# Optimization experiments

Hardware: AMD Instinct MI355X
Metric: run time of the kernel (lower is better)

## Reference

```python
import jax, jax.numpy as jnp
import numpy as np

# GeoFormer.generate_proposal constants (cfg.threshold_ins, cfg.min_pts_num,
# instance classes start at semantic id 4 on ScanNet)
THRESHOLD = 0.5
MIN_PTS_NUM = 50
MIN_INST_CLASS = 4


def setup_inputs() -> dict:
    key = jax.random.key(0)
    k1, k2, k3, k4 = jax.random.split(key, 4)
    B, Q, N, C = 4, 128, 50000, 20
    mask_logits = jax.random.normal(k1, (B, Q, N), dtype=jnp.float32)
    cls_logits = jax.random.normal(k2, (B, Q, C), dtype=jnp.float32)
    seg_pred = jax.random.randint(k3, (B, N), 0, C, dtype=jnp.int64)
    fg_idxs = jax.random.randint(k4, (B * N,), 0, 300000, dtype=jnp.int64)
    return {"mask_logits": mask_logits, "cls_logits": cls_logits,
            "seg_pred": seg_pred, "fg_idxs": fg_idxs}


def reference(mask_logits, cls_logits, seg_pred, fg_idxs):
    # mask_logits: [B, Q, N]  per-query point-mask logits (dense form of the
    #   per-batch list in the original; batch_offsets become the B dim)
    # cls_logits:  [B, Q, C]  per-query class logits
    # seg_pred:    [B, N]     per-point semantic prediction
    # fg_idxs:     [B*N]      foreground -> original point id map
    B, Q, N = mask_logits.shape
    m = jax.nn.sigmoid(mask_logits)                         # [B, Q, N]
    cls_pred = jnp.argmax(cls_logits, axis=2)               # [B, Q]

    # (mask_logit_b[n] > threshold) & (seg_pred == cls_logits_pred[b, n])
    sel = (m > THRESHOLD) & (seg_pred[:, None, :] == cls_pred[:, :, None])  # [B,Q,N]
    cnt = sel.sum(axis=-1)                                  # [B, Q] proposal sizes

    # score = mean of sigmoid over selected points
    msel = jnp.where(sel, m, jnp.zeros((), m.dtype))
    scores = msel.sum(axis=-1) / jnp.maximum(cnt, 1).astype(m.dtype)  # [B, Q]

    # skip if too few points or a background/wall class (< 4)
    valid = (cnt >= MIN_PTS_NUM) & (cls_pred >= MIN_INST_CLASS)       # [B, Q]

    proposal_masks = sel & valid[:, :, None]                # dense proposal_idx
    scores = jnp.where(valid, scores, jnp.zeros((), scores.dtype))
    global_ids = fg_idxs.reshape(B, N)                      # fg_idxs remap per point
    return proposal_masks, scores, valid, cls_pred, global_ids
```

## Files before the change

### kernel.cpp

```cpp
#include <hip/hip_runtime.h>
#include <math.h>

#define BB 4
#define QQ 128
#define NN 50000
#define CC 20
#define ROWS (BB * QQ)
#define NV4 (NN / 4)
#define TPB 256
#define BPR 4
#define QUOTA (NV4 / BPR)
#define FULL_ITERS 12
#define TAIL 53
#define THRESH_CNT 50
#define MIN_CLS 4

typedef float f32x4 __attribute__((ext_vector_type(4)));
typedef int   i32x4 __attribute__((ext_vector_type(4)));

struct Ws {
    float sum[ROWS];
    int   cnt[ROWS];
    int   cls[ROWS];
    int   valid[ROWS];
};

__global__ void k0_argmax_zero(const float* __restrict__ cls_logits, Ws* ws) {
    int r = blockIdx.x * blockDim.x + threadIdx.x;
    if (r >= ROWS) return;
    const float* p = cls_logits + r * CC;
    float best = p[0];
    int bi = 0;
    #pragma unroll
    for (int c = 1; c < CC; ++c) {
        float v = p[c];
        if (v > best) { best = v; bi = c; }
    }
    ws->cls[r] = bi;
    ws->sum[r] = 0.0f;
    ws->cnt[r] = 0;
}

__global__ __launch_bounds__(256) void k1_select(
        const float* __restrict__ mask_logits,
        const int*   __restrict__ seg_pred,
        float* __restrict__ out_mask,
        Ws* __restrict__ ws) {
    const int row = blockIdx.y;
    const int b   = row >> 7;
    const int cls = ws->cls[row];
    const int off = blockIdx.x * QUOTA;

    const f32x4* __restrict__ ml = (const f32x4*)(mask_logits + (size_t)row * NN) + off;
    const i32x4* __restrict__ sp = (const i32x4*)(seg_pred + b * NN) + off;
    f32x4* __restrict__ om = (f32x4*)(out_mask + (size_t)row * NN) + off;

    const int t = threadIdx.x;

    float lsum = 0.0f;
    int   lcnt = 0;

    f32x4 v0[4]; i32x4 s0v[4];
    #pragma unroll
    for (int j = 0; j < 4; ++j) {
        v0[j]  = ml[t + j * TPB];
        s0v[j] = sp[t + j * TPB];
    }

    #pragma unroll
    for (int bat = 0; bat < 3; ++bat) {
        f32x4 nv[4]; i32x4 ns[4];
        if (bat < 2) {
            const int nbase = (bat + 1) * (4 * TPB) + t;
            #pragma unroll
            for (int j = 0; j < 4; ++j) {
                nv[j] = ml[nbase + j * TPB];
                ns[j] = sp[nbase + j * TPB];
            }
        }
        const int base = bat * (4 * TPB) + t;
        #pragma unroll
        for (int j = 0; j < 4; ++j) {
            f32x4 vv = v0[j];
            i32x4 ss = s0v[j];
            bool c0 = (vv.x > 0.0f) & (ss.x == cls);
            bool c1 = (vv.y > 0.0f) & (ss.y == cls);
            bool c2 = (vv.z > 0.0f) & (ss.z == cls);
            bool c3 = (vv.w > 0.0f) & (ss.w == cls);
            float g0 = 1.0f / (1.0f + __expf(-vv.x));
            float g1 = 1.0f / (1.0f + __expf(-vv.y));
            float g2 = 1.0f / (1.0f + __expf(-vv.z));
            float g3 = 1.0f / (1.0f + __expf(-vv.w));
            f32x4 o;
            o.x = c0 ? 1.0f : 0.0f;
            o.y = c1 ? 1.0f : 0.0f;
            o.z = c2 ? 1.0f : 0.0f;
            o.w = c3 ? 1.0f : 0.0f;
            lsum += (c0 ? g0 : 0.0f) + (c1 ? g1 : 0.0f)
                  + (c2 ? g2 : 0.0f) + (c3 ? g3 : 0.0f);
            lcnt += (int)c0 + (int)c1 + (int)c2 + (int)c3;
            __builtin_nontemporal_store(o, &om[base + j * TPB]);
        }
        #pragma unroll
        for (int j = 0; j < 4; ++j) { v0[j] = nv[j]; s0v[j] = ns[j]; }
    }

    if (t < TAIL) {
        const int idx = FULL_ITERS * TPB + t;
        f32x4 vv = ml[idx];
        i32x4 ss = sp[idx];
        bool c0 = (vv.x > 0.0f) & (ss.x == cls);
        bool c1 = (vv.y > 0.0f) & (ss.y == cls);
        bool c2 = (vv.z > 0.0f) & (ss.z == cls);
        bool c3 = (vv.w > 0.0f) & (ss.w == cls);
        float g0 = 1.0f / (1.0f + __expf(-vv.x));
        float g1 = 1.0f / (1.0f + __expf(-vv.y));
        float g2 = 1.0f / (1.0f + __expf(-vv.z));
        float g3 = 1.0f / (1.0f + __expf(-vv.w));
        f32x4 o;
        o.x = c0 ? 1.0f : 0.0f;
        o.y = c1 ? 1.0f : 0.0f;
        o.z = c2 ? 1.0f : 0.0f;
        o.w = c3 ? 1.0f : 0.0f;
        lsum += (c0 ? g0 : 0.0f) + (c1 ? g1 : 0.0f)
              + (c2 ? g2 : 0.0f) + (c3 ? g3 : 0.0f);
        lcnt += (int)c0 + (int)c1 + (int)c2 + (int)c3;
        __builtin_nontemporal_store(o, &om[idx]);
    }

    #pragma unroll
    for (int offr = 32; offr > 0; offr >>= 1) {
        lsum += __shfl_down(lsum, offr);
        lcnt += __shfl_down(lcnt, offr);
    }
    __shared__ float ssum[4];
    __shared__ int   scnt[4];
    const int wave = threadIdx.x >> 6;
    const int lane = threadIdx.x & 63;
    if (lane == 0) { ssum[wave] = lsum; scnt[wave] = lcnt; }
    __syncthreads();
    if (threadIdx.x == 0) {
        float ts = ssum[0] + ssum[1] + ssum[2] + ssum[3];
        int   tc = scnt[0] + scnt[1] + scnt[2] + scnt[3];
        atomicAdd(&ws->sum[row], ts);
        atomicAdd(&ws->cnt[row], tc);
    }
}

__global__ void k2_finalize_gids(const int* __restrict__ fg,
                                 float* __restrict__ out,
                                 Ws* __restrict__ ws) {
    const int idx = blockIdx.x * blockDim.x + threadIdx.x;
    if (idx < ROWS) {
        int   cnt = ws->cnt[idx];
        int   cls = ws->cls[idx];
        float sum = ws->sum[idx];
        int valid = (cnt >= THRESH_CNT) && (cls >= MIN_CLS);
        ws->valid[idx] = valid;
        float* tail = out + (size_t)ROWS * NN;
        tail[idx]            = valid ? (sum / (float)max(cnt, 1)) : 0.0f;
        tail[ROWS + idx]     = valid ? 1.0f : 0.0f;
        tail[2 * ROWS + idx] = (float)cls;
    }
    const int nv4 = (BB * NN) / 4;
    if (idx < nv4) {
        float* gids = out + (size_t)ROWS * NN + 3 * ROWS;
        i32x4 v = ((const i32x4*)fg)[idx];
        f32x4 o;
        o.x = (float)v.x; o.y = (float)v.y; o.z = (float)v.z; o.w = (float)v.w;
        __builtin_nontemporal_store(o, &((f32x4*)gids)[idx]);
    }
}

__global__ __launch_bounds__(256) void k3_fixup(
        float* __restrict__ out_mask, const Ws* __restrict__ ws) {
    const int row = blockIdx.y;
    if (ws->valid[row]) return;
    f32x4* __restrict__ om = (f32x4*)(out_mask + (size_t)row * NN)
                             + blockIdx.x * QUOTA;
    const f32x4 z = {0.0f, 0.0f, 0.0f, 0.0f};
    const int t = threadIdx.x;
    #pragma unroll
    for (int i = 0; i < FULL_ITERS; ++i)
        __builtin_nontemporal_store(z, &om[t + i * TPB]);
    if (t < TAIL)
        __builtin_nontemporal_store(z, &om[FULL_ITERS * TPB + t]);
}

extern "C" void kernel_launch(void* const* d_in, const int* in_sizes, int n_in,
                              void* d_out, int out_size, void* d_ws, size_t ws_size,
                              hipStream_t stream) {
    const float* mask_logits = (const float*)d_in[0];
    const float* cls_logits  = (const float*)d_in[1];
    const int*   seg_pred    = (const int*)d_in[2];
    const int*   fg_idxs     = (const int*)d_in[3];

    float* out = (float*)d_out;
    Ws* ws = (Ws*)d_ws;

    float* out_mask = out;

    k0_argmax_zero<<<(ROWS + 255) / 256, 256, 0, stream>>>(cls_logits, ws);

    dim3 g1(BPR, ROWS);
    k1_select<<<g1, TPB, 0, stream>>>(mask_logits, seg_pred, out_mask, ws);

    const int gids_blocks = ((BB * NN) / 4 + 255) / 256;
    k2_finalize_gids<<<gids_blocks, 256, 0, stream>>>(fg_idxs, out, ws);

    k3_fixup<<<g1, TPB, 0, stream>>>(out_mask, ws);
}
```

Baseline: 204.4 us.

## Compact selection masks to ballot bitmasks and write final masks once

The first pass now computes the argmax inline, produces per-wave ballot bitmasks of the selection in workspace, and stores per-block partial sums instead of using atomics. A second pass reads the bits and the validity flag and writes the full float mask exactly once. This removes the dense write followed by a zero-fixup rewrite for invalid rows, and the separate argmax launch. It depends on the workspace being large enough, and otherwise falls back to the old path. Nontemporal stores are replaced by plain stores.

```diff
diff --git a/kernel.cpp b/kernel.cpp
--- a/kernel.cpp
+++ b/kernel.cpp
@@ -14,9 +14,20 @@
 #define TAIL 53
 #define THRESH_CNT 50
 #define MIN_CLS 4
+#define NITER 13
 
 typedef float f32x4 __attribute__((ext_vector_type(4)));
 typedef int   i32x4 __attribute__((ext_vector_type(4)));
+typedef unsigned long long u64;
+typedef unsigned long long u64x2 __attribute__((ext_vector_type(2)));
+
+struct Ws2 {
+    float psum[ROWS][BPR];
+    int   pcnt[ROWS][BPR];
+    int   cls[ROWS];
+    int   valid[ROWS];
+    u64   bits[(size_t)ROWS * BPR * NITER * 16];
+};
 
 struct Ws {
     float sum[ROWS];
@@ -25,84 +36,63 @@
     int   valid[ROWS];
 };
 
-__global__ void k0_argmax_zero(const float* __restrict__ cls_logits, Ws* ws) {
-    int r = blockIdx.x * blockDim.x + threadIdx.x;
-    if (r >= ROWS) return;
-    const float* p = cls_logits + r * CC;
-    float best = p[0];
-    int bi = 0;
-    #pragma unroll
-    for (int c = 1; c < CC; ++c) {
-        float v = p[c];
-        if (v > best) { best = v; bi = c; }
-    }
-    ws->cls[r] = bi;
-    ws->sum[r] = 0.0f;
-    ws->cnt[r] = 0;
-}
-
-__global__ __launch_bounds__(256) void k1_select(
+
+__global__ __launch_bounds__(256) void k1a_reduce_bits(
         const float* __restrict__ mask_logits,
         const int*   __restrict__ seg_pred,
-        float* __restrict__ out_mask,
-        Ws* __restrict__ ws) {
+        const float* __restrict__ cls_logits,
+        Ws2* __restrict__ ws) {
     const int row = blockIdx.y;
     const int b   = row >> 7;
-    const int cls = ws->cls[row];
-    const int off = blockIdx.x * QUOTA;
+    const int bx  = blockIdx.x;
+    const int off = bx * QUOTA;
+
+    const float* cp = cls_logits + row * CC;
+    float best = cp[0];
+    int cls = 0;
+    #pragma unroll
+    for (int c = 1; c < CC; ++c) {
+        float v = cp[c];
+        if (v > best) { best = v; cls = c; }
+    }
 
     const f32x4* __restrict__ ml = (const f32x4*)(mask_logits + (size_t)row * NN) + off;
     const i32x4* __restrict__ sp = (const i32x4*)(seg_pred + b * NN) + off;
-    f32x4* __restrict__ om = (f32x4*)(out_mask + (size_t)row * NN) + off;
+    u64* __restrict__ wbits = ws->bits + (size_t)(row * BPR + bx) * NITER * 16;
 
     const int t = threadIdx.x;
+    const int wave = t >> 6;
+    const int lane = t & 63;
 
     float lsum = 0.0f;
     int   lcnt = 0;
 
-    f32x4 v0[4]; i32x4 s0v[4];
-    #pragma unroll
-    for (int j = 0; j < 4; ++j) {
-        v0[j]  = ml[t + j * TPB];
-        s0v[j] = sp[t + j * TPB];
-    }
-
-    #pragma unroll
-    for (int bat = 0; bat < 3; ++bat) {
-        f32x4 nv[4]; i32x4 ns[4];
-        if (bat < 2) {
-            const int nbase = (bat + 1) * (4 * TPB) + t;
-            #pragma unroll
-            for (int j = 0; j < 4; ++j) {
-                nv[j] = ml[nbase + j * TPB];
-                ns[j] = sp[nbase + j * TPB];
-            }
+    #pragma unroll 4
+    for (int i = 0; i < FULL_ITERS; ++i) {
+        f32x4 vv = ml[i * TPB + t];
+        i32x4 ss = sp[i * TPB + t];
+        bool c0 = (vv.x > 0.0f) & (ss.x == cls);
+        bool c1 = (vv.y > 0.0f) & (ss.y == cls);
+        bool c2 = (vv.z > 0.0f) & (ss.z == cls);
+        bool c3 = (vv.w > 0.0f) & (ss.w == cls);
+        float g0 = 1.0f / (1.0f + __expf(-vv.x));
+        float g1 = 1.0f / (1.0f + __expf(-vv.y));
+        float g2 = 1.0f / (1.0f + __expf(-vv.z));
+        float g3 = 1.0f / (1.0f + __expf(-vv.w));
+        lsum += (c0 ? g0 : 0.0f) + (c1 ? g1 : 0.0f)
+              + (c2 ? g2 : 0.0f) + (c3 ? g3 : 0.0f);
+        lcnt += (int)c0 + (int)c1 + (int)c2 + (int)c3;
+        u64 b0 = __ballot(c0);
+        u64 b1 = __ballot(c1);
+        u64 b2 = __ballot(c2);
+        u64 b3 = __ballot(c3);
+        if (lane == 0) {
+            u64x2* dst = (u64x2*)(wbits + (size_t)(i * 4 + wave) * 4);
+            u64x2 q0; q0.x = b0; q0.y = b1;
+            u64x2 q1; q1.x = b2; q1.y = b3;
+            dst[0] = q0;
+            dst[1] = q1;
         }
-        const int base = bat * (4 * TPB) + t;
-        #pragma unroll
-        for (int j = 0; j < 4; ++j) {
-            f32x4 vv = v0[j];
-            i32x4 ss = s0v[j];
-            bool c0 = (vv.x > 0.0f) & (ss.x == cls);
-            bool c1 = (vv.y > 0.0f) & (ss.y == cls);
-            bool c2 = (vv.z > 0.0f) & (ss.z == cls);
-            bool c3 = (vv.w > 0.0f) & (ss.w == cls);
-            float g0 = 1.0f / (1.0f + __expf(-vv.x));
-            float g1 = 1.0f / (1.0f + __expf(-vv.y));
-            float g2 = 1.0f / (1.0f + __expf(-vv.z));
-            float g3 = 1.0f / (1.0f + __expf(-vv.w));
-            f32x4 o;
-            o.x = c0 ? 1.0f : 0.0f;
-            o.y = c1 ? 1.0f : 0.0f;
-            o.z = c2 ? 1.0f : 0.0f;
-            o.w = c3 ? 1.0f : 0.0f;
-            lsum += (c0 ? g0 : 0.0f) + (c1 ? g1 : 0.0f)
-                  + (c2 ? g2 : 0.0f) + (c3 ? g3 : 0.0f);
-            lcnt += (int)c0 + (int)c1 + (int)c2 + (int)c3;
-            __builtin_nontemporal_store(o, &om[base + j * TPB]);
-        }
-        #pragma unroll
-        for (int j = 0; j < 4; ++j) { v0[j] = nv[j]; s0v[j] = ns[j]; }
     }
 
     if (t < TAIL) {
@@ -117,15 +107,168 @@
         float g1 = 1.0f / (1.0f + __expf(-vv.y));
         float g2 = 1.0f / (1.0f + __expf(-vv.z));
         float g3 = 1.0f / (1.0f + __expf(-vv.w));
-        f32x4 o;
-        o.x = c0 ? 1.0f : 0.0f;
-        o.y = c1 ? 1.0f : 0.0f;
-        o.z = c2 ? 1.0f : 0.0f;
-        o.w = c3 ? 1.0f : 0.0f;
         lsum += (c0 ? g0 : 0.0f) + (c1 ? g1 : 0.0f)
               + (c2 ? g2 : 0.0f) + (c3 ? g3 : 0.0f);
         lcnt += (int)c0 + (int)c1 + (int)c2 + (int)c3;
-        __builtin_nontemporal_store(o, &om[idx]);
+        u64 b0 = __ballot(c0);
+        u64 b1 = __ballot(c1);
+        u64 b2 = __ballot(c2);
+        u64 b3 = __ballot(c3);
+        if (lane == 0) {
+            u64x2* dst = (u64x2*)(wbits + (size_t)(FULL_ITERS * 4 + 0) * 4);
+            u64x2 q0; q0.x = b0; q0.y = b1;
+            u64x2 q1; q1.x = b2; q1.y = b3;
+            dst[0] = q0;
+            dst[1] = q1;
+        }
+    }
+
+    #pragma unroll
+    for (int offr = 32; offr > 0; offr >>= 1) {
+        lsum += __shfl_down(lsum, offr);
+        lcnt += __shfl_down(lcnt, offr);
+    }
+    __shared__ float ssum[4];
+    __shared__ int   scnt[4];
+    if (lane == 0) { ssum[wave] = lsum; scnt[wave] = lcnt; }
+    __syncthreads();
+    if (t == 0) {
+        ws->psum[row][bx] = ssum[0] + ssum[1] + ssum[2] + ssum[3];
+        ws->pcnt[row][bx] = scnt[0] + scnt[1] + scnt[2] + scnt[3];
+        if (bx == 0) ws->cls[row] = cls;
+    }
+}
+
+__global__ void k2_finalize_new(const int* __restrict__ fg,
+                                float* __restrict__ out,
+                                Ws2* __restrict__ ws) {
+    const int idx = blockIdx.x * blockDim.x + threadIdx.x;
+    if (idx < ROWS) {
+        float sum = ws->psum[idx][0] + ws->psum[idx][1]
+                  + ws->psum[idx][2] + ws->psum[idx][3];
+        int   cnt = ws->pcnt[idx][0] + ws->pcnt[idx][1]
+                  + ws->pcnt[idx][2] + ws->pcnt[idx][3];
+        int   cls = ws->cls[idx];
+        int valid = (cnt >= THRESH_CNT) && (cls >= MIN_CLS);
+        ws->valid[idx] = valid;
+        float* tail = out + (size_t)ROWS * NN;
+        tail[idx]            = valid ? (sum / (float)max(cnt, 1)) : 0.0f;
+        tail[ROWS + idx]     = valid ? 1.0f : 0.0f;
+        tail[2 * ROWS + idx] = (float)cls;
+    }
+    const int nv4 = (BB * NN) / 4;
+    if (idx < nv4) {
+        float* gids = out + (size_t)ROWS * NN + 3 * ROWS;
+        i32x4 v = ((const i32x4*)fg)[idx];
+        f32x4 o;
+        o.x = (float)v.x; o.y = (float)v.y; o.z = (float)v.z; o.w = (float)v.w;
+        ((f32x4*)gids)[idx] = o;
+    }
+}
+
+__global__ __launch_bounds__(256) void k1b_store(
+        float* __restrict__ out_mask, const Ws2* __restrict__ ws) {
+    const int row = blockIdx.y;
+    const int bx  = blockIdx.x;
+    const float validf = ws->valid[row] ? 1.0f : 0.0f;
+
+    f32x4* __restrict__ om = (f32x4*)(out_mask + (size_t)row * NN) + bx * QUOTA;
+    const u64* __restrict__ wbits =
+        ws->bits + (size_t)(row * BPR + bx) * NITER * 16;
+
+    const int t = threadIdx.x;
+    const int wave = t >> 6;
+    const int lane = t & 63;
+
+    #pragma unroll 4
+    for (int i = 0; i < FULL_ITERS; ++i) {
+        const u64x2* pb = (const u64x2*)(wbits + (size_t)(i * 4 + wave) * 4);
+        u64x2 q0 = pb[0];
+        u64x2 q1 = pb[1];
+        f32x4 o;
+        o.x = ((q0.x >> lane) & 1ull) ? validf : 0.0f;
+        o.y = ((q0.y >> lane) & 1ull) ? validf : 0.0f;
+        o.z = ((q1.x >> lane) & 1ull) ? validf : 0.0f;
+        o.w = ((q1.y >> lane) & 1ull) ? validf : 0.0f;
+        om[i * TPB + t] = o;
+    }
+    if (t < TAIL) {
+        const u64x2* pb = (const u64x2*)(wbits + (size_t)(FULL_ITERS * 4) * 4);
+        u64x2 q0 = pb[0];
+        u64x2 q1 = pb[1];
+        f32x4 o;
+        o.x = ((q0.x >> lane) & 1ull) ? validf : 0.0f;
+        o.y = ((q0.y >> lane) & 1ull) ? validf : 0.0f;
+        o.z = ((q1.x >> lane) & 1ull) ? validf : 0.0f;
+        o.w = ((q1.y >> lane) & 1ull) ? validf : 0.0f;
+        om[FULL_ITERS * TPB + t] = o;
+    }
+}
+
+
+__global__ void k0_argmax_zero(const float* __restrict__ cls_logits, Ws* ws) {
+    int r = blockIdx.x * blockDim.x + threadIdx.x;
+    if (r >= ROWS) return;
+    const float* p = cls_logits + r * CC;
+    float best = p[0];
+    int bi = 0;
+    #pragma unroll
+    for (int c = 1; c < CC; ++c) {
+        float v = p[c];
+        if (v > best) { best = v; bi = c; }
+    }
+    ws->cls[r] = bi;
+    ws->sum[r] = 0.0f;
+    ws->cnt[r] = 0;
+}
+
+__device__ __forceinline__ void proc4(const f32x4 vv, const i32x4 ss,
+                                      const int cls, float& lsum, int& lcnt,
+                                      f32x4* __restrict__ dst) {
+    bool c0 = (vv.x > 0.0f) & (ss.x == cls);
+    bool c1 = (vv.y > 0.0f) & (ss.y == cls);
+    bool c2 = (vv.z > 0.0f) & (ss.z == cls);
+    bool c3 = (vv.w > 0.0f) & (ss.w == cls);
+    float g0 = 1.0f / (1.0f + __expf(-vv.x));
+    float g1 = 1.0f / (1.0f + __expf(-vv.y));
+    float g2 = 1.0f / (1.0f + __expf(-vv.z));
+    float g3 = 1.0f / (1.0f + __expf(-vv.w));
+    f32x4 o;
+    o.x = c0 ? 1.0f : 0.0f;
+    o.y = c1 ? 1.0f : 0.0f;
+    o.z = c2 ? 1.0f : 0.0f;
+    o.w = c3 ? 1.0f : 0.0f;
+    lsum += (c0 ? g0 : 0.0f) + (c1 ? g1 : 0.0f)
+          + (c2 ? g2 : 0.0f) + (c3 ? g3 : 0.0f);
+    lcnt += (int)c0 + (int)c1 + (int)c2 + (int)c3;
+    *dst = o;
+}
+
+__global__ __launch_bounds__(256) void k1_select(
+        const float* __restrict__ mask_logits,
+        const int*   __restrict__ seg_pred,
+        float* __restrict__ out_mask,
+        Ws* __restrict__ ws) {
+    const int row = blockIdx.y;
+    const int b   = row >> 7;
+    const int cls = ws->cls[row];
+    const int off = blockIdx.x * QUOTA;
+
+    const f32x4* __restrict__ ml = (const f32x4*)(mask_logits + (size_t)row * NN) + off;
+    const i32x4* __restrict__ sp = (const i32x4*)(seg_pred + b * NN) + off;
+    f32x4* __restrict__ om = (f32x4*)(out_mask + (size_t)row * NN) + off;
+
+    const int t = threadIdx.x;
+    float lsum = 0.0f;
+    int   lcnt = 0;
+
+    #pragma unroll 4
+    for (int i = 0; i < FULL_ITERS; ++i)
+        proc4(ml[i * TPB + t], sp[i * TPB + t], cls, lsum, lcnt,
+              &om[i * TPB + t]);
+    if (t < TAIL) {
+        const int idx = FULL_ITERS * TPB + t;
+        proc4(ml[idx], sp[idx], cls, lsum, lcnt, &om[idx]);
     }
 
     #pragma unroll
@@ -140,10 +283,8 @@
     if (lane == 0) { ssum[wave] = lsum; scnt[wave] = lcnt; }
     __syncthreads();
     if (threadIdx.x == 0) {
-        float ts = ssum[0] + ssum[1] + ssum[2] + ssum[3];
-        int   tc = scnt[0] + scnt[1] + scnt[2] + scnt[3];
-        atomicAdd(&ws->sum[row], ts);
-        atomicAdd(&ws->cnt[row], tc);
+        atomicAdd(&ws->sum[row], ssum[0] + ssum[1] + ssum[2] + ssum[3]);
+        atomicAdd(&ws->cnt[row], scnt[0] + scnt[1] + scnt[2] + scnt[3]);
     }
 }
 
@@ -168,7 +309,7 @@
         i32x4 v = ((const i32x4*)fg)[idx];
         f32x4 o;
         o.x = (float)v.x; o.y = (float)v.y; o.z = (float)v.z; o.w = (float)v.w;
-        __builtin_nontemporal_store(o, &((f32x4*)gids)[idx]);
+        ((f32x4*)gids)[idx] = o;
     }
 }
 
@@ -182,10 +323,11 @@
     const int t = threadIdx.x;
     #pragma unroll
     for (int i = 0; i < FULL_ITERS; ++i)
-        __builtin_nontemporal_store(z, &om[t + i * TPB]);
+        om[t + i * TPB] = z;
     if (t < TAIL)
-        __builtin_nontemporal_store(z, &om[FULL_ITERS * TPB + t]);
-}
+        om[FULL_ITERS * TPB + t] = z;
+}
+
 
 extern "C" void kernel_launch(void* const* d_in, const int* in_sizes, int n_in,
                               void* d_out, int out_size, void* d_ws, size_t ws_size,
@@ -196,17 +338,22 @@
     const int*   fg_idxs     = (const int*)d_in[3];
 
     float* out = (float*)d_out;
-    Ws* ws = (Ws*)d_ws;
-
     float* out_mask = out;
 
-    k0_argmax_zero<<<(ROWS + 255) / 256, 256, 0, stream>>>(cls_logits, ws);
-
+    const int gids_blocks = ((BB * NN) / 4 + 255) / 256;
     dim3 g1(BPR, ROWS);
-    k1_select<<<g1, TPB, 0, stream>>>(mask_logits, seg_pred, out_mask, ws);
-
-    const int gids_blocks = ((BB * NN) / 4 + 255) / 256;
-    k2_finalize_gids<<<gids_blocks, 256, 0, stream>>>(fg_idxs, out, ws);
-
-    k3_fixup<<<g1, TPB, 0, stream>>>(out_mask, ws);
-}
+
+    if (ws_size >= sizeof(Ws2)) {
+        Ws2* ws = (Ws2*)d_ws;
+        k1a_reduce_bits<<<g1, TPB, 0, stream>>>(mask_logits, seg_pred,
+                                                cls_logits, ws);
+        k2_finalize_new<<<gids_blocks, 256, 0, stream>>>(fg_idxs, out, ws);
+        k1b_store<<<g1, TPB, 0, stream>>>(out_mask, ws);
+    } else {
+        Ws* ws = (Ws*)d_ws;
+        k0_argmax_zero<<<(ROWS + 255) / 256, 256, 0, stream>>>(cls_logits, ws);
+        k1_select<<<g1, TPB, 0, stream>>>(mask_logits, seg_pred, out_mask, ws);
+        k2_finalize_gids<<<gids_blocks, 256, 0, stream>>>(fg_idxs, out, ws);
+        k3_fixup<<<g1, TPB, 0, stream>>>(out_mask, ws);
+    }
+}
```

Result: faster. 200.3 us (-2.0%).

## Fuse argmax, selection, finalize and fixup into one row-per-block kernel

Applied to the files above, without the earlier changes.

Each row of the mask is now handled by a single 1024-thread block. It computes the class argmax itself, reduces count and sum across the block, and decides validity before writing the mask. Selection bits are held in a 64-bit register per thread, so the mask is written once with validity already applied. This removes the workspace atomics, two kernel launches and the second zeroing pass over invalid rows. In exchange, stores wait until the block-wide reduction finishes, and with 512 large blocks occupancy and load/store overlap may suffer.

```diff
diff --git a/kernel.cpp b/kernel.cpp
--- a/kernel.cpp
+++ b/kernel.cpp
@@ -7,106 +7,62 @@
 #define CC 20
 #define ROWS (BB * QQ)
 #define NV4 (NN / 4)
-#define TPB 256
-#define BPR 4
-#define QUOTA (NV4 / BPR)
-#define FULL_ITERS 12
-#define TAIL 53
+#define TPB1 1024
+#define FULL1 12
+#define TAIL1 212
 #define THRESH_CNT 50
 #define MIN_CLS 4
 
 typedef float f32x4 __attribute__((ext_vector_type(4)));
 typedef int   i32x4 __attribute__((ext_vector_type(4)));
+typedef unsigned long long u64;
 
-struct Ws {
-    float sum[ROWS];
-    int   cnt[ROWS];
-    int   cls[ROWS];
-    int   valid[ROWS];
-};
+__global__ __launch_bounds__(1024) void k1_fused(
+        const float* __restrict__ mask_logits,
+        const int*   __restrict__ seg_pred,
+        const float* __restrict__ cls_logits,
+        float* __restrict__ out) {
+    const int row = blockIdx.x;
+    const int b   = row >> 7;
 
-__global__ void k0_argmax_zero(const float* __restrict__ cls_logits, Ws* ws) {
-    int r = blockIdx.x * blockDim.x + threadIdx.x;
-    if (r >= ROWS) return;
-    const float* p = cls_logits + r * CC;
-    float best = p[0];
-    int bi = 0;
+    const float* cp = cls_logits + row * CC;
+    float best = cp[0];
+    int cls = 0;
     #pragma unroll
     for (int c = 1; c < CC; ++c) {
-        float v = p[c];
-        if (v > best) { best = v; bi = c; }
+        float v = cp[c];
+        if (v > best) { best = v; cls = c; }
     }
-    ws->cls[r] = bi;
-    ws->sum[r] = 0.0f;
-    ws->cnt[r] = 0;
-}
 
-__global__ __launch_bounds__(256) void k1_select(
-        const float* __restrict__ mask_logits,
-        const int*   __restrict__ seg_pred,
-        float* __restrict__ out_mask,
-        Ws* __restrict__ ws) {
-    const int row = blockIdx.y;
-    const int b   = row >> 7;
-    const int cls = ws->cls[row];
-    const int off = blockIdx.x * QUOTA;
-
-    const f32x4* __restrict__ ml = (const f32x4*)(mask_logits + (size_t)row * NN) + off;
-    const i32x4* __restrict__ sp = (const i32x4*)(seg_pred + b * NN) + off;
-    f32x4* __restrict__ om = (f32x4*)(out_mask + (size_t)row * NN) + off;
+    const f32x4* __restrict__ ml = (const f32x4*)(mask_logits + (size_t)row * NN);
+    const i32x4* __restrict__ sp = (const i32x4*)(seg_pred + b * NN);
+    f32x4* __restrict__ om = (f32x4*)(out + (size_t)row * NN);
 
     const int t = threadIdx.x;
-
+    u64   bits = 0;
     float lsum = 0.0f;
     int   lcnt = 0;
 
-    f32x4 v0[4]; i32x4 s0v[4];
-    #pragma unroll
-    for (int j = 0; j < 4; ++j) {
-        v0[j]  = ml[t + j * TPB];
-        s0v[j] = sp[t + j * TPB];
+    #pragma unroll 4
+    for (int i = 0; i < FULL1; ++i) {
+        f32x4 vv = ml[i * TPB1 + t];
+        i32x4 ss = sp[i * TPB1 + t];
+        bool c0 = (vv.x > 0.0f) & (ss.x == cls);
+        bool c1 = (vv.y > 0.0f) & (ss.y == cls);
+        bool c2 = (vv.z > 0.0f) & (ss.z == cls);
+        bool c3 = (vv.w > 0.0f) & (ss.w == cls);
+        float g0 = 1.0f / (1.0f + __expf(-vv.x));
+        float g1 = 1.0f / (1.0f + __expf(-vv.y));
+        float g2 = 1.0f / (1.0f + __expf(-vv.z));
+        float g3 = 1.0f / (1.0f + __expf(-vv.w));
+        lsum += (c0 ? g0 : 0.0f) + (c1 ? g1 : 0.0f)
+              + (c2 ? g2 : 0.0f) + (c3 ? g3 : 0.0f);
+        lcnt += (int)c0 + (int)c1 + (int)c2 + (int)c3;
+        u64 nib = (u64)c0 | ((u64)c1 << 1) | ((u64)c2 << 2) | ((u64)c3 << 3);
+        bits |= nib << (4 * i);
     }
-
-    #pragma unroll
-    for (int bat = 0; bat < 3; ++bat) {
-        f32x4 nv[4]; i32x4 ns[4];
-        if (bat < 2) {
-            const int nbase = (bat + 1) * (4 * TPB) + t;
-            #pragma unroll
-            for (int j = 0; j < 4; ++j) {
-                nv[j] = ml[nbase + j * TPB];
-                ns[j] = sp[nbase + j * TPB];
-            }
-        }
-        const int base = bat * (4 * TPB) + t;
-        #pragma unroll
-        for (int j = 0; j < 4; ++j) {
-            f32x4 vv = v0[j];
-            i32x4 ss = s0v[j];
-            bool c0 = (vv.x > 0.0f) & (ss.x == cls);
-            bool c1 = (vv.y > 0.0f) & (ss.y == cls);
-            bool c2 = (vv.z > 0.0f) & (ss.z == cls);
-            bool c3 = (vv.w > 0.0f) & (ss.w == cls);
-            float g0 = 1.0f / (1.0f + __expf(-vv.x));
-            float g1 = 1.0f / (1.0f + __expf(-vv.y));
-            float g2 = 1.0f / (1.0f + __expf(-vv.z));
-            float g3 = 1.0f / (1.0f + __expf(-vv.w));
-            f32x4 o;
-            o.x = c0 ? 1.0f : 0.0f;
-            o.y = c1 ? 1.0f : 0.0f;
-            o.z = c2 ? 1.0f : 0.0f;
-            o.w = c3 ? 1.0f : 0.0f;
-            lsum += (c0 ? g0 : 0.0f) + (c1 ? g1 : 0.0f)
-                  + (c2 ? g2 : 0.0f) + (c3 ? g3 : 0.0f);
-            lcnt += (int)c0 + (int)c1 + (int)c2 + (int)c3;
-            __builtin_nontemporal_store(o, &om[base + j * TPB]);
-        }
-        #pragma unroll
-        for (int j = 0; j < 4; ++j) { v0[j] = nv[j]; s0v[j] = ns[j]; }
-    }
-
-    if (t < TAIL) {
-        const int idx = FULL_ITERS * TPB + t;
+    if (t < TAIL1) {
+        const int idx = FULL1 * TPB1 + t;
         f32x4 vv = ml[idx];
         i32x4 ss = sp[idx];
         bool c0 = (vv.x > 0.0f) & (ss.x == cls);
@@ -117,15 +73,11 @@
         float g1 = 1.0f / (1.0f + __expf(-vv.y));
         float g2 = 1.0f / (1.0f + __expf(-vv.z));
         float g3 = 1.0f / (1.0f + __expf(-vv.w));
-        f32x4 o;
-        o.x = c0 ? 1.0f : 0.0f;
-        o.y = c1 ? 1.0f : 0.0f;
-        o.z = c2 ? 1.0f : 0.0f;
-        o.w = c3 ? 1.0f : 0.0f;
         lsum += (c0 ? g0 : 0.0f) + (c1 ? g1 : 0.0f)
               + (c2 ? g2 : 0.0f) + (c3 ? g3 : 0.0f);
         lcnt += (int)c0 + (int)c1 + (int)c2 + (int)c3;
-        __builtin_nontemporal_store(o, &om[idx]);
+        u64 nib = (u64)c0 | ((u64)c1 << 1) | ((u64)c2 << 2) | ((u64)c3 << 3);
+        bits |= nib << (4 * FULL1);
     }
 
     #pragma unroll
@@ -133,35 +85,49 @@
         lsum += __shfl_down(lsum, offr);
         lcnt += __shfl_down(lcnt, offr);
     }
-    __shared__ float ssum[4];
-    __shared__ int   scnt[4];
-    const int wave = threadIdx.x >> 6;
-    const int lane = threadIdx.x & 63;
+    __shared__ float ssum[16];
+    __shared__ int   scnt[16];
+    const int wave = t >> 6;
+    const int lane = t & 63;
     if (lane == 0) { ssum[wave] = lsum; scnt[wave] = lcnt; }
     __syncthreads();
-    if (threadIdx.x == 0) {
-        float ts = ssum[0] + ssum[1] + ssum[2] + ssum[3];
-        int   tc = scnt[0] + scnt[1] + scnt[2] + scnt[3];
-        atomicAdd(&ws->sum[row], ts);
-        atomicAdd(&ws->cnt[row], tc);
+    float sum = 0.0f;
+    int   cnt = 0;
+    #pragma unroll
+    for (int w = 0; w < 16; ++w) { sum += ssum[w]; cnt += scnt[w]; }
+    const bool  valid  = (cnt >= THRESH_CNT) && (cls >= MIN_CLS);
+    const float validf = valid ? 1.0f : 0.0f;
+
+    if (t == 0) {
+        float* tail = out + (size_t)ROWS * NN;
+        tail[row]            = valid ? (sum / (float)max(cnt, 1)) : 0.0f;
+        tail[ROWS + row]     = validf;
+        tail[2 * ROWS + row] = (float)cls;
+    }
+
+    #pragma unroll 4
+    for (int i = 0; i < FULL1; ++i) {
+        u64 nib = bits >> (4 * i);
+        f32x4 o;
+        o.x = (nib & 1ull) ? validf : 0.0f;
+        o.y = (nib & 2ull) ? validf : 0.0f;
+        o.z = (nib & 4ull) ? validf : 0.0f;
+        o.w = (nib & 8ull) ? validf : 0.0f;
+        __builtin_nontemporal_store(o, &om[i * TPB1 + t]);
+    }
+    if (t < TAIL1) {
+        u64 nib = bits >> (4 * FULL1);
+        f32x4 o;
+        o.x = (nib & 1ull) ? validf : 0.0f;
+        o.y = (nib & 2ull) ? validf : 0.0f;
+        o.z = (nib & 4ull) ? validf : 0.0f;
+        o.w = (nib & 8ull) ? validf : 0.0f;
+        __builtin_nontemporal_store(o, &om[FULL1 * TPB1 + t]);
     }
 }
 
-__global__ void k2_finalize_gids(const int* __restrict__ fg,
-                                 float* __restrict__ out,
-                                 Ws* __restrict__ ws) {
+__global__ void k2_gids(const int* __restrict__ fg, float* __restrict__ out) {
     const int idx = blockIdx.x * blockDim.x + threadIdx.x;
-    if (idx < ROWS) {
-        int   cnt = ws->cnt[idx];
-        int   cls = ws->cls[idx];
-        float sum = ws->sum[idx];
-        int valid = (cnt >= THRESH_CNT) && (cls >= MIN_CLS);
-        ws->valid[idx] = valid;
-        float* tail = out + (size_t)ROWS * NN;
-        tail[idx]            = valid ? (sum / (float)max(cnt, 1)) : 0.0f;
-        tail[ROWS + idx]     = valid ? 1.0f : 0.0f;
-        tail[2 * ROWS + idx] = (float)cls;
-    }
     const int nv4 = (BB * NN) / 4;
     if (idx < nv4) {
         float* gids = out + (size_t)ROWS * NN + 3 * ROWS;
@@ -170,21 +136,6 @@
         o.x = (float)v.x; o.y = (float)v.y; o.z = (float)v.z; o.w = (float)v.w;
         __builtin_nontemporal_store(o, &((f32x4*)gids)[idx]);
     }
-}
-
-__global__ __launch_bounds__(256) void k3_fixup(
-        float* __restrict__ out_mask, const Ws* __restrict__ ws) {
-    const int row = blockIdx.y;
-    if (ws->valid[row]) return;
-    f32x4* __restrict__ om = (f32x4*)(out_mask + (size_t)row * NN)
-                             + blockIdx.x * QUOTA;
-    const f32x4 z = {0.0f, 0.0f, 0.0f, 0.0f};
-    const int t = threadIdx.x;
-    #pragma unroll
-    for (int i = 0; i < FULL_ITERS; ++i)
-        __builtin_nontemporal_store(z, &om[t + i * TPB]);
-    if (t < TAIL)
-        __builtin_nontemporal_store(z, &om[FULL_ITERS * TPB + t]);
 }
 
 extern "C" void kernel_launch(void* const* d_in, const int* in_sizes, int n_in,
@@ -196,17 +147,10 @@
     const int*   fg_idxs     = (const int*)d_in[3];
 
     float* out = (float*)d_out;
-    Ws* ws = (Ws*)d_ws;
+    (void)d_ws; (void)ws_size;
 
-    float* out_mask = out;
-
-    k0_argmax_zero<<<(ROWS + 255) / 256, 256, 0, stream>>>(cls_logits, ws);
-
-    dim3 g1(BPR, ROWS);
-    k1_select<<<g1, TPB, 0, stream>>>(mask_logits, seg_pred, out_mask, ws);
+    k1_fused<<<ROWS, TPB1, 0, stream>>>(mask_logits, seg_pred, cls_logits, out);
 
     const int gids_blocks = ((BB * NN) / 4 + 255) / 256;
-    k2_finalize_gids<<<gids_blocks, 256, 0, stream>>>(fg_idxs, out, ws);
-
-    k3_fixup<<<g1, TPB, 0, stream>>>(out_mask, ws);
+    k2_gids<<<gids_blocks, 256, 0, stream>>>(fg_idxs, out);
 }
```

Measured after the change: 190.3 us. 6.9% less time.
